# Kernel tuning notes

Measured on AMD Instinct MI355X. Metric: run time of the kernel, lower is better.

Reference implementation:

```python
import jax, jax.numpy as jnp
import numpy as np

N = 50000        # vertices
E = 1_600_000    # edges (avg degree 32)
CIN = 8          # in_channels (scalar input features)
COUT = 32        # out_channels (tangent vector channels, complex -> trailing dim 2)
R = 2            # n_corr_rings (radial profile rings)
EPS = 1e-6


def setup_inputs() -> dict:
    key = jax.random.key(0)
    ks = jax.random.split(key, 12)
    x = jax.random.normal(ks[0], (N, CIN), jnp.float32)
    edge_index = jax.random.randint(ks[1], (2, E), 0, N, dtype=jnp.int32)
    # precomputed per-edge transport * radial interpolation coefficients (re, im) per ring
    pcmp_gather = jax.random.normal(ks[2], (E, R, 2), jnp.float32)
    # TransField learned radial profile and phase offset (offset=True)
    W_rad = jax.random.normal(ks[3], (R, CIN, COUT), jnp.float32) / np.float32(np.sqrt(R * CIN))
    phase = jax.random.normal(ks[4], (COUT,), jnp.float32)
    # TangentNonLin bias after the field conv
    b_nl = jax.random.normal(ks[5], (COUT,), jnp.float32) * 0.1
    # three TangentPerceptrons: complex-linear (real weight shared over re/im) + TangentNonLin
    sc = np.float32(1.0 / np.sqrt(COUT))
    W1 = jax.random.normal(ks[6], (COUT, COUT), jnp.float32) * sc
    b1 = jax.random.normal(ks[7], (COUT,), jnp.float32) * 0.1
    W2 = jax.random.normal(ks[8], (COUT, COUT), jnp.float32) * sc
    b2 = jax.random.normal(ks[9], (COUT,), jnp.float32) * 0.1
    W3 = jax.random.normal(ks[10], (COUT, COUT), jnp.float32) * sc
    b3 = jax.random.normal(ks[11], (COUT,), jnp.float32) * 0.1
    return dict(x=x, edge_index=edge_index, pcmp_gather=pcmp_gather, W_rad=W_rad,
                phase=phase, b_nl=b_nl, W1=W1, b1=b1, W2=W2, b2=b2, W3=W3, b3=b3)


def tangent_nonlin(z, b):
    # ReLU on magnitude with learned per-channel bias, phase preserved
    mag = jnp.sqrt(jnp.sum(z * z, axis=-1) + EPS)           # [N, C]
    scale = jax.nn.relu(mag + b) / mag                      # [N, C]
    return z * scale[..., None]


def trans_field(x, src, dst, pcmp_gather, W_rad, phase, n_nodes):
    xs = x[src]                                             # gather: [E, CIN]
    t = jnp.einsum('ei,rio->ero', xs, W_rad)                # [E, R, COUT]
    # modulate by complex transport coeffs per ring, sum rings -> [E, COUT, 2]
    msg = jnp.sum(t[..., None] * pcmp_gather[:, :, None, :], axis=1)
    agg = jax.ops.segment_sum(msg, dst, num_segments=n_nodes)  # scatter: [N, COUT, 2]
    # learned phase offset: rotate each output channel by e^{i*phase}
    c, s = jnp.cos(phase), jnp.sin(phase)
    re = agg[..., 0] * c - agg[..., 1] * s
    im = agg[..., 0] * s + agg[..., 1] * c
    return jnp.stack([re, im], axis=-1)                     # [N, COUT, 2]


def reference(x, edge_index, pcmp_gather, W_rad, phase, b_nl, W1, b1, W2, b2, W3, b3):
    src, dst = edge_index[0], edge_index[1]
    y = trans_field(x, src, dst, pcmp_gather, W_rad, phase, x.shape[0])
    y = tangent_nonlin(y, b_nl)
    for W, b in ((W1, b1), (W2, b2), (W3, b3)):
        y = jnp.einsum('nik,io->nok', y, W)                 # complex-linear (shared real weight)
        y = tangent_nonlin(y, b)
    return y
```

## Files before the change

kernel.cpp:

```cpp
#include <hip/hip_runtime.h>

#define CIN 8
#define COUT 32
#define NR 2
#define EPSF 1e-6f

#define BSH 5
#define BNODES 32
#define NBMAX 2048
#define CHUNK 8192
#define IDBITS 21
#define IDMASK ((1u << IDBITS) - 1u)
#define SRCMASK 0x03FFFFFFu
#define PSTAGE 1792
#define AREG (PSTAGE / 256)

__global__ __launch_bounds__(256) void bucket_hist(
    const int* __restrict__ eidx, int* __restrict__ bucketCnt, int E, int nb)
{
    __shared__ int cnt[NBMAX];
    for (int i = threadIdx.x; i < nb; i += 256) cnt[i] = 0;
    __syncthreads();
    for (int e = blockIdx.x * 256 + threadIdx.x; e < E; e += gridDim.x * 256)
        atomicAdd(&cnt[eidx[E + e] >> BSH], 1);
    __syncthreads();
    for (int i = threadIdx.x; i < nb; i += 256)
        if (cnt[i]) atomicAdd(&bucketCnt[i], cnt[i]);
}

__global__ __launch_bounds__(1024) void scan_init(
    const int* __restrict__ bucketCnt, int* __restrict__ bucketBase,
    int* __restrict__ gCursor, int nb)
{
    __shared__ int sA[NBMAX], sB[NBMAX];
    for (int i = threadIdx.x; i < NBMAX; i += 1024)
        sA[i] = (i < nb) ? bucketCnt[i] : 0;
    __syncthreads();
    int* src = sA; int* dst = sB;
    for (int off = 1; off < NBMAX; off <<= 1) {
        for (int i = threadIdx.x; i < NBMAX; i += 1024)
            dst[i] = src[i] + (i >= off ? src[i - off] : 0);
        __syncthreads();
        int* tmp = src; src = dst; dst = tmp;
    }
    for (int i = threadIdx.x; i < nb; i += 1024) {
        int incl = src[i];
        int base = incl - bucketCnt[i];
        bucketBase[i] = base;
        gCursor[i] = base;
        if (i == nb - 1) bucketBase[nb] = incl;
    }
}

template<bool PACKED>
__global__ __launch_bounds__(256) void binify(
    const int* __restrict__ eidx, int* __restrict__ gCursor,
    unsigned* __restrict__ outMeta,
    float4*   __restrict__ pcmpS,
    const float* __restrict__ pcmp, int E, int nb)
{
    __shared__ int cnt[NBMAX];
    __shared__ int sA[NBMAX], sB[NBMAX];
    __shared__ int gbase[NBMAX];
    __shared__ unsigned sid[CHUNK];
    __shared__ unsigned short bucketOf[CHUNK];

    const int e0 = blockIdx.x * CHUNK;
    const int num = min(CHUNK, E - e0);

    for (int i = threadIdx.x; i < nb; i += 256) cnt[i] = 0;
    __syncthreads();
    for (int k = threadIdx.x; k < num; k += 256)
        atomicAdd(&cnt[eidx[E + e0 + k] >> BSH], 1);
    __syncthreads();

    for (int j = threadIdx.x; j < NBMAX; j += 256) sA[j] = (j < nb) ? cnt[j] : 0;
    __syncthreads();
    int* src = sA; int* dstp = sB;
    for (int off = 1; off < NBMAX; off <<= 1) {
        for (int j = threadIdx.x; j < NBMAX; j += 256)
            dstp[j] = src[j] + (j >= off ? src[j - off] : 0);
        __syncthreads();
        int* tmp = src; src = dstp; dstp = tmp;
    }

    for (int b = threadIdx.x; b < nb; b += 256)
        gbase[b] = atomicAdd(&gCursor[b], cnt[b]);
    __syncthreads();
    for (int i = threadIdx.x; i < nb; i += 256) cnt[i] = 0;
    __syncthreads();

    for (int k = threadIdx.x; k < num; k += 256) {
        int e = e0 + k;
        int d = eidx[E + e];
        int b = d >> BSH;
        int slot = (b ? src[b - 1] : 0) + atomicAdd(&cnt[b], 1);
        sid[slot] = ((unsigned)(d & (BNODES - 1)) << IDBITS) | (unsigned)e;
        bucketOf[slot] = (unsigned short)b;
    }
    __syncthreads();

    for (int s = threadIdx.x; s < num; s += 256) {
        int b = bucketOf[s];
        int intra = s - (b ? src[b - 1] : 0);
        unsigned v = sid[s];
        int pos = gbase[b] + intra;
        if (PACKED) {
            int id = v & IDMASK;
            unsigned dl = v >> IDBITS;
            unsigned sv = (unsigned)eidx[id];
            outMeta[pos] = (dl << 26) | sv;
            pcmpS[pos] = *reinterpret_cast<const float4*>(pcmp + (size_t)id * 4);
        } else {
            outMeta[pos] = v;
        }
    }
}

template<bool SRC16>
__global__ __launch_bounds__(256) void fused_team_kernel(
    const float* __restrict__ x,
    const float4* __restrict__ pcmpS,
    const unsigned* __restrict__ meta,
    const int* __restrict__ bucketBase,
    const float* __restrict__ W_rad, const float* __restrict__ phase,
    const float* __restrict__ b_nl,
    const float* __restrict__ W1, const float* __restrict__ b1,
    const float* __restrict__ W2, const float* __restrict__ b2,
    const float* __restrict__ W3, const float* __restrict__ b3,
    float* __restrict__ out, int N)
{
    __shared__ float sWrad[NR * CIN][COUT];
    __shared__ float sPh[COUT][2];
    __shared__ float sBias[4][COUT];
    __shared__ float4 pcL[PSTAGE];
    __shared__ unsigned short srcL16[SRC16 ? PSTAGE : 2];
    __shared__ unsigned srcL32[SRC16 ? 2 : PSTAGE];
    __shared__ float Qbuf[BNODES][33];
    __shared__ int cnt[BNODES], segS[BNODES], padL[BNODES], cur[BNODES];
    __shared__ int totPad;

    for (int i = threadIdx.x; i < NR * CIN * COUT; i += 256) ((float*)sWrad)[i] = W_rad[i];
    if (threadIdx.x < COUT) {
        float sn, cs; __sincosf(phase[threadIdx.x], &sn, &cs);
        sPh[threadIdx.x][0] = cs; sPh[threadIdx.x][1] = sn;
        sBias[0][threadIdx.x] = b_nl[threadIdx.x];
        sBias[1][threadIdx.x] = b1[threadIdx.x];
        sBias[2][threadIdx.x] = b2[threadIdx.x];
        sBias[3][threadIdx.x] = b3[threadIdx.x];
    }
    if (threadIdx.x < BNODES) cnt[threadIdx.x] = 0;

    const int start = bucketBase[blockIdx.x];
    const int total = bucketBase[blockIdx.x + 1] - start;
    const bool ovf0 = (total > PSTAGE);
    if (threadIdx.x == 0) totPad = ovf0 ? 0x7FFFFFFF : 0;
    __syncthreads();

    unsigned mreg[AREG];
    float4   preg[AREG];
    const int staged = ovf0 ? 0 : total;
#pragma unroll
    for (int kk = 0; kk < AREG; ++kk) {
        int k = threadIdx.x + (kk << 8);
        if (k < staged) {
            mreg[kk] = meta[start + k];
            preg[kk] = pcmpS[start + k];
            atomicAdd(&cnt[mreg[kk] >> 26], 1);
        }
    }
    __syncthreads();

    if (threadIdx.x < BNODES) {
        int v = cnt[threadIdx.x];
        int m = v;
        m = max(m, __shfl_xor(m, 1, 32));
        m = max(m, __shfl_xor(m, 2, 32));
        m = max(m, __shfl_xor(m, 4, 32));
        int pl = m;
        int incl = pl;
#pragma unroll
        for (int off = 1; off < BNODES; off <<= 1) {
            int u = __shfl_up(incl, off, 32);
            if ((int)threadIdx.x >= off) incl += u;
        }
        segS[threadIdx.x] = incl - pl;
        cur[threadIdx.x]  = incl - pl;
        padL[threadIdx.x] = pl;
        if (threadIdx.x == BNODES - 1 && !ovf0) totPad = incl;
    }
    __syncthreads();

    const bool fb = (totPad > PSTAGE);

    if (!fb) {
#pragma unroll
        for (int kk = 0; kk < AREG; ++kk) {
            int k = threadIdx.x + (kk << 8);
            if (k < staged) {
                unsigned m = mreg[kk];
                int pos = atomicAdd(&cur[m >> 26], 1);
                if (SRC16) srcL16[pos] = (unsigned short)(m & 0xFFFFu);
                else       srcL32[pos] = m & SRCMASK;
                pcL[pos] = preg[kk];
            }
        }
        if (threadIdx.x < BNODES) {
            int p0 = segS[threadIdx.x] + cnt[threadIdx.x];
            int p1 = segS[threadIdx.x] + padL[threadIdx.x];
            float4 z = {0.f, 0.f, 0.f, 0.f};
            for (int p = p0; p < p1; ++p) {
                if (SRC16) srcL16[p] = 0; else srcL32[p] = 0;
                pcL[p] = z;
            }
        }
    }
    __syncthreads();

    const int c    = threadIdx.x & 31;
    const int sub  = threadIdx.x >> 5;
    const int team = c >> 3;
    const int il   = c & 7;
    const int gl   = sub * 4 + team;
    const int node0 = blockIdx.x << BSH;

    float4 qa = {0.f, 0.f, 0.f, 0.f};
    if (!fb) {
        const int base = segS[gl];
        const int T = padL[gl];
#pragma unroll 4
        for (int t = 0; t < T; ++t) {
            int sv = SRC16 ? (int)srcL16[base + t] : (int)srcL32[base + t];
            float4 pc4 = pcL[base + t];
            float xf = x[(sv << 3) + il];
            qa.x += xf * pc4.x;
            qa.y += xf * pc4.y;
            qa.z += xf * pc4.z;
            qa.w += xf * pc4.w;
        }
    } else {
        const float4* pcG = pcmpS + start;
        for (int t = 0; t < total; ++t) {
            unsigned m = meta[start + t];
            if ((int)(m >> 26) == gl) {
                float4 pc4 = pcG[t];
                float xf = x[(size_t)(m & SRCMASK) * CIN + il];
                qa.x += xf * pc4.x;
                qa.y += xf * pc4.y;
                qa.z += xf * pc4.z;
                qa.w += xf * pc4.w;
            }
        }
    }

    Qbuf[gl][2 * il]      = qa.x;
    Qbuf[gl][2 * il + 1]  = qa.y;
    Qbuf[gl][16 + 2 * il] = qa.z;
    Qbuf[gl][17 + 2 * il] = qa.w;

    const float* __restrict__ Wt0 = W1;
    const float* __restrict__ Wt1 = W2;
    const float* __restrict__ Wt2 = W3;
#pragma unroll
    for (int r = 0; r < 4; ++r) {
        const int gln = sub * 4 + r;
        const int n   = node0 + gln;
        float a0 = 0.f, a1 = 0.f;
#pragma unroll
        for (int ri = 0; ri < NR * CIN; ++ri) {
            float w = sWrad[ri][c];
            a0 += w * Qbuf[gln][2 * ri];
            a1 += w * Qbuf[gln][2 * ri + 1];
        }
        float cs = sPh[c][0], sn = sPh[c][1];
        float re = a0 * cs - a1 * sn;
        float im = a0 * sn + a1 * cs;
        float mag = sqrtf(re * re + im * im + EPSF);
        float sc  = fmaxf(mag + sBias[0][c], 0.f) / mag;
        re *= sc; im *= sc;
#pragma unroll
        for (int L = 0; L < 3; ++L) {
            const float* __restrict__ Wl = (L == 0) ? Wt0 : (L == 1) ? Wt1 : Wt2;
            float bb0 = 0.f, bb1 = 0.f;
#pragma unroll
            for (int i = 0; i < COUT; ++i) {
                float w = Wl[i * COUT + c];
                bb0 += w * __shfl(re, i, 32);
                bb1 += w * __shfl(im, i, 32);
            }
            float m2 = sqrtf(bb0 * bb0 + bb1 * bb1 + EPSF);
            float s2 = fmaxf(m2 + sBias[L + 1][c], 0.f) / m2;
            re = bb0 * s2; im = bb1 * s2;
        }
        if (n < N) {
            float2 v; v.x = re; v.y = im;
            *reinterpret_cast<float2*>(out + ((n << 6) + (c << 1))) = v;
        }
    }
}

__global__ __launch_bounds__(256) void fused_bucket_fallback(
    const float* __restrict__ x, const int* __restrict__ eidx,
    const float* __restrict__ pcmp, const int* __restrict__ bucketBase,
    const unsigned* __restrict__ sorted,
    const float* __restrict__ W_rad, const float* __restrict__ phase,
    const float* __restrict__ b_nl,
    const float* __restrict__ W1, const float* __restrict__ b1,
    const float* __restrict__ W2, const float* __restrict__ b2,
    const float* __restrict__ W3, const float* __restrict__ b3,
    float* __restrict__ out, int N)
{
    __shared__ float Q[BNODES][COUT];
    __shared__ float sWrad[NR * CIN][COUT];
    __shared__ float sW[3][COUT][COUT];
    __shared__ float sPh[COUT][2];
    __shared__ float sBias[4][COUT];

    for (int i = threadIdx.x; i < BNODES * COUT; i += 256) ((float*)Q)[i] = 0.f;
    for (int i = threadIdx.x; i < NR * CIN * COUT; i += 256) ((float*)sWrad)[i] = W_rad[i];
    for (int i = threadIdx.x; i < COUT * COUT; i += 256) {
        ((float*)sW[0])[i] = W1[i];
        ((float*)sW[1])[i] = W2[i];
        ((float*)sW[2])[i] = W3[i];
    }
    if (threadIdx.x < COUT) {
        float sn, cs; __sincosf(phase[threadIdx.x], &sn, &cs);
        sPh[threadIdx.x][0] = cs; sPh[threadIdx.x][1] = sn;
        sBias[0][threadIdx.x] = b_nl[threadIdx.x];
        sBias[1][threadIdx.x] = b1[threadIdx.x];
        sBias[2][threadIdx.x] = b2[threadIdx.x];
        sBias[3][threadIdx.x] = b3[threadIdx.x];
    }
    __syncthreads();

    const int c   = threadIdx.x & 31;
    const int sub = threadIdx.x >> 5;
    const int i_idx  = (c >> 1) & 7;
    const int pc_off = ((c >> 4) << 1) | (c & 1);
    const int start = bucketBase[blockIdx.x];
    const int end   = bucketBase[blockIdx.x + 1];

    for (int p = start + sub; p < end; p += 8) {
        unsigned v0 = sorted[p];
        int id0 = v0 & IDMASK;
        int s0 = eidx[id0];
        atomicAdd(&Q[v0 >> IDBITS][c],
                  x[(size_t)s0 * CIN + i_idx] * pcmp[(size_t)id0 * 4 + pc_off]);
    }
    __syncthreads();

    const int node0 = blockIdx.x << BSH;
#pragma unroll
    for (int r = 0; r < 4; ++r) {
        const int gl = r * 8 + sub;
        const int n  = node0 + gl;
        float a0 = 0.f, a1 = 0.f;
#pragma unroll
        for (int ri = 0; ri < NR * CIN; ++ri) {
            float w = sWrad[ri][c];
            a0 += w * Q[gl][2 * ri];
            a1 += w * Q[gl][2 * ri + 1];
        }
        float cs = sPh[c][0], sn = sPh[c][1];
        float re = a0 * cs - a1 * sn;
        float im = a0 * sn + a1 * cs;
        float mag = sqrtf(re * re + im * im + EPSF);
        float sc  = fmaxf(mag + sBias[0][c], 0.f) / mag;
        re *= sc; im *= sc;
#pragma unroll
        for (int L = 0; L < 3; ++L) {
            float b0 = 0.f, b1v = 0.f;
#pragma unroll
            for (int i = 0; i < COUT; ++i) {
                float w = sW[L][i][c];
                b0  += w * __shfl(re, i, 32);
                b1v += w * __shfl(im, i, 32);
            }
            float m2 = sqrtf(b0 * b0 + b1v * b1v + EPSF);
            float s2 = fmaxf(m2 + sBias[L + 1][c], 0.f) / m2;
            re = b0 * s2; im = b1v * s2;
        }
        if (n < N) {
            float2 v; v.x = re; v.y = im;
            *reinterpret_cast<float2*>(out + ((size_t)n * COUT + c) * 2) = v;
        }
    }
}

extern "C" void kernel_launch(void* const* d_in, const int* in_sizes, int n_in,
                              void* d_out, int out_size, void* d_ws, size_t ws_size,
                              hipStream_t stream)
{
    const float* x     = (const float*)d_in[0];
    const int*   eidx  = (const int*)  d_in[1];
    const float* pcmp  = (const float*)d_in[2];
    const float* W_rad = (const float*)d_in[3];
    const float* phase = (const float*)d_in[4];
    const float* b_nl  = (const float*)d_in[5];
    const float* W1    = (const float*)d_in[6];
    const float* b1    = (const float*)d_in[7];
    const float* W2    = (const float*)d_in[8];
    const float* b2    = (const float*)d_in[9];
    const float* W3    = (const float*)d_in[10];
    const float* b3    = (const float*)d_in[11];
    float* out = (float*)d_out;

    const int N = in_sizes[0] / CIN;
    const int E = in_sizes[1] / 2;
    const int nb = (N + BNODES - 1) >> BSH;
    const int nchunk = (E + CHUNK - 1) / CHUNK;

    float4*   pcmpS      = (float4*)d_ws;
    unsigned* meta       = (unsigned*)(pcmpS + E);
    int*      bucketCnt  = (int*)(meta + E);
    int*      bucketBase = bucketCnt + NBMAX;
    int*      gCursor    = bucketBase + NBMAX + 1;
    size_t needed = (size_t)((char*)(gCursor + NBMAX) - (char*)d_ws);

    if (ws_size >= needed) {
        hipMemsetAsync(bucketCnt, 0, (size_t)nb * sizeof(int), stream);
        bucket_hist<<<256, 256, 0, stream>>>(eidx, bucketCnt, E, nb);
        scan_init<<<1, 1024, 0, stream>>>(bucketCnt, bucketBase, gCursor, nb);
        binify<true><<<nchunk, 256, 0, stream>>>(eidx, gCursor, meta, pcmpS, pcmp, E, nb);
        if (N <= 65536) {
            fused_team_kernel<true><<<nb, 256, 0, stream>>>(
                x, pcmpS, meta, bucketBase,
                W_rad, phase, b_nl, W1, b1, W2, b2, W3, b3, out, N);
        } else {
            fused_team_kernel<false><<<nb, 256, 0, stream>>>(
                x, pcmpS, meta, bucketBase,
                W_rad, phase, b_nl, W1, b1, W2, b2, W3, b3, out, N);
        }
    } else {
        int*      bc = (int*)d_ws;
        int*      bb = bc + NBMAX;
        int*      gc = bb + NBMAX + 1;
        unsigned* so = (unsigned*)(gc + NBMAX);
        hipMemsetAsync(bc, 0, (size_t)nb * sizeof(int), stream);
        bucket_hist<<<256, 256, 0, stream>>>(eidx, bc, E, nb);
        scan_init<<<1, 1024, 0, stream>>>(bc, bb, gc, nb);
        binify<false><<<nchunk, 256, 0, stream>>>(eidx, gc, so, nullptr, pcmp, E, nb);
        fused_bucket_fallback<<<nb, 256, 0, stream>>>(
            x, eidx, pcmp, bb, so,
            W_rad, phase, b_nl, W1, b1, W2, b2, W3, b3, out, N);
    }
}
```

Measured before the change: 182.9 us.

## Stage only packed indices in LDS and read pcmp from global to raise occupancy

The fused kernel no longer stages the float4 transport coefficients in shared memory or registers. It stores a packed (source, original-offset) word per sorted edge and reads pcmpS from global memory inside the aggregation loop, masking padded iterations instead of zero-filling padding. This cuts LDS use and register pressure so that launch_bounds(256,6) can keep more blocks resident, at the cost of scattered global float4 reads within a bucket. The binify kernel also moves to 512 threads with half-size chunks, which doubles the number of blocks.

After: 170.6 us. 6.7% less time.

```diff
diff --git a/kernel.cpp b/kernel.cpp
--- a/kernel.cpp
+++ b/kernel.cpp
@@ -8,7 +8,8 @@
 #define BSH 5
 #define BNODES 32
 #define NBMAX 2048
-#define CHUNK 8192
+#define CHUNK 4096
+#define BINT 512
 #define IDBITS 21
 #define IDMASK ((1u << IDBITS) - 1u)
 #define SRCMASK 0x03FFFFFFu
@@ -53,7 +54,7 @@
 }
 
 template<bool PACKED>
-__global__ __launch_bounds__(256) void binify(
+__global__ __launch_bounds__(BINT) void binify(
     const int* __restrict__ eidx, int* __restrict__ gCursor,
     unsigned* __restrict__ outMeta,
     float4*   __restrict__ pcmpS,
@@ -68,29 +69,29 @@
     const int e0 = blockIdx.x * CHUNK;
     const int num = min(CHUNK, E - e0);
 
-    for (int i = threadIdx.x; i < nb; i += 256) cnt[i] = 0;
-    __syncthreads();
-    for (int k = threadIdx.x; k < num; k += 256)
+    for (int i = threadIdx.x; i < nb; i += BINT) cnt[i] = 0;
+    __syncthreads();
+    for (int k = threadIdx.x; k < num; k += BINT)
         atomicAdd(&cnt[eidx[E + e0 + k] >> BSH], 1);
     __syncthreads();
 
-    for (int j = threadIdx.x; j < NBMAX; j += 256) sA[j] = (j < nb) ? cnt[j] : 0;
+    for (int j = threadIdx.x; j < NBMAX; j += BINT) sA[j] = (j < nb) ? cnt[j] : 0;
     __syncthreads();
     int* src = sA; int* dstp = sB;
     for (int off = 1; off < NBMAX; off <<= 1) {
-        for (int j = threadIdx.x; j < NBMAX; j += 256)
+        for (int j = threadIdx.x; j < NBMAX; j += BINT)
             dstp[j] = src[j] + (j >= off ? src[j - off] : 0);
         __syncthreads();
         int* tmp = src; src = dstp; dstp = tmp;
     }
 
-    for (int b = threadIdx.x; b < nb; b += 256)
+    for (int b = threadIdx.x; b < nb; b += BINT)
         gbase[b] = atomicAdd(&gCursor[b], cnt[b]);
     __syncthreads();
-    for (int i = threadIdx.x; i < nb; i += 256) cnt[i] = 0;
-    __syncthreads();
-
-    for (int k = threadIdx.x; k < num; k += 256) {
+    for (int i = threadIdx.x; i < nb; i += BINT) cnt[i] = 0;
+    __syncthreads();
+
+    for (int k = threadIdx.x; k < num; k += BINT) {
         int e = e0 + k;
         int d = eidx[E + e];
         int b = d >> BSH;
@@ -100,7 +101,7 @@
     }
     __syncthreads();
 
-    for (int s = threadIdx.x; s < num; s += 256) {
+    for (int s = threadIdx.x; s < num; s += BINT) {
         int b = bucketOf[s];
         int intra = s - (b ? src[b - 1] : 0);
         unsigned v = sid[s];
@@ -118,7 +119,7 @@
 }
 
 template<bool SRC16>
-__global__ __launch_bounds__(256) void fused_team_kernel(
+__global__ __launch_bounds__(256, 6) void fused_team_kernel(
     const float* __restrict__ x,
     const float4* __restrict__ pcmpS,
     const unsigned* __restrict__ meta,
@@ -133,12 +134,10 @@
     __shared__ float sWrad[NR * CIN][COUT];
     __shared__ float sPh[COUT][2];
     __shared__ float sBias[4][COUT];
-    __shared__ float4 pcL[PSTAGE];
-    __shared__ unsigned short srcL16[SRC16 ? PSTAGE : 2];
-    __shared__ unsigned srcL32[SRC16 ? 2 : PSTAGE];
+    __shared__ unsigned srtPk[PSTAGE];
+    __shared__ unsigned short srtK[SRC16 ? 2 : PSTAGE];
     __shared__ float Qbuf[BNODES][33];
     __shared__ int cnt[BNODES], segS[BNODES], padL[BNODES], cur[BNODES];
-    __shared__ int totPad;
 
     for (int i = threadIdx.x; i < NR * CIN * COUT; i += 256) ((float*)sWrad)[i] = W_rad[i];
     if (threadIdx.x < COUT) {
@@ -153,19 +152,16 @@
 
     const int start = bucketBase[blockIdx.x];
     const int total = bucketBase[blockIdx.x + 1] - start;
-    const bool ovf0 = (total > PSTAGE);
-    if (threadIdx.x == 0) totPad = ovf0 ? 0x7FFFFFFF : 0;
+    const bool fb = (total > PSTAGE);
     __syncthreads();
 
     unsigned mreg[AREG];
-    float4   preg[AREG];
-    const int staged = ovf0 ? 0 : total;
+    const int staged = fb ? 0 : total;
 #pragma unroll
     for (int kk = 0; kk < AREG; ++kk) {
         int k = threadIdx.x + (kk << 8);
         if (k < staged) {
             mreg[kk] = meta[start + k];
-            preg[kk] = pcmpS[start + k];
             atomicAdd(&cnt[mreg[kk] >> 26], 1);
         }
     }
@@ -177,21 +173,17 @@
         m = max(m, __shfl_xor(m, 1, 32));
         m = max(m, __shfl_xor(m, 2, 32));
         m = max(m, __shfl_xor(m, 4, 32));
-        int pl = m;
-        int incl = pl;
+        int incl = v;
 #pragma unroll
         for (int off = 1; off < BNODES; off <<= 1) {
             int u = __shfl_up(incl, off, 32);
             if ((int)threadIdx.x >= off) incl += u;
         }
-        segS[threadIdx.x] = incl - pl;
-        cur[threadIdx.x]  = incl - pl;
-        padL[threadIdx.x] = pl;
-        if (threadIdx.x == BNODES - 1 && !ovf0) totPad = incl;
-    }
-    __syncthreads();
-
-    const bool fb = (totPad > PSTAGE);
+        segS[threadIdx.x] = incl - v;
+        cur[threadIdx.x]  = incl - v;
+        padL[threadIdx.x] = m;
+    }
+    __syncthreads();
 
     if (!fb) {
 #pragma unroll
@@ -200,18 +192,12 @@
             if (k < staged) {
                 unsigned m = mreg[kk];
                 int pos = atomicAdd(&cur[m >> 26], 1);
-                if (SRC16) srcL16[pos] = (unsigned short)(m & 0xFFFFu);
-                else       srcL32[pos] = m & SRCMASK;
-                pcL[pos] = preg[kk];
-            }
-        }
-        if (threadIdx.x < BNODES) {
-            int p0 = segS[threadIdx.x] + cnt[threadIdx.x];
-            int p1 = segS[threadIdx.x] + padL[threadIdx.x];
-            float4 z = {0.f, 0.f, 0.f, 0.f};
-            for (int p = p0; p < p1; ++p) {
-                if (SRC16) srcL16[p] = 0; else srcL32[p] = 0;
-                pcL[p] = z;
+                if (SRC16) {
+                    srtPk[pos] = ((unsigned)k << 16) | (m & 0xFFFFu);
+                } else {
+                    srtPk[pos] = m & SRCMASK;
+                    srtK[pos] = (unsigned short)k;
+                }
             }
         }
     }
@@ -226,13 +212,23 @@
 
     float4 qa = {0.f, 0.f, 0.f, 0.f};
     if (!fb) {
-        const int base = segS[gl];
-        const int T = padL[gl];
+        const int base  = segS[gl];
+        const int myCnt = cnt[gl];
+        const int Tw    = padL[gl];
+        const int last  = total - 1;
 #pragma unroll 4
-        for (int t = 0; t < T; ++t) {
-            int sv = SRC16 ? (int)srcL16[base + t] : (int)srcL32[base + t];
-            float4 pc4 = pcL[base + t];
-            float xf = x[(sv << 3) + il];
+        for (int t = 0; t < Tw; ++t) {
+            bool act = (t < myCnt);
+            int slot = min(base + t, last);
+            int sv, kk2;
+            if (SRC16) {
+                unsigned p = srtPk[slot];
+                sv = (int)(p & 0xFFFFu); kk2 = (int)(p >> 16);
+            } else {
+                sv = (int)srtPk[slot]; kk2 = (int)srtK[slot];
+            }
+            float4 pc4 = pcmpS[start + kk2];
+            float xf = act ? x[(sv << 3) + il] : 0.f;
             qa.x += xf * pc4.x;
             qa.y += xf * pc4.y;
             qa.z += xf * pc4.z;
@@ -258,9 +254,6 @@
     Qbuf[gl][16 + 2 * il] = qa.z;
     Qbuf[gl][17 + 2 * il] = qa.w;
 
-    const float* __restrict__ Wt0 = W1;
-    const float* __restrict__ Wt1 = W2;
-    const float* __restrict__ Wt2 = W3;
 #pragma unroll
     for (int r = 0; r < 4; ++r) {
         const int gln = sub * 4 + r;
@@ -280,7 +273,7 @@
         re *= sc; im *= sc;
 #pragma unroll
         for (int L = 0; L < 3; ++L) {
-            const float* __restrict__ Wl = (L == 0) ? Wt0 : (L == 1) ? Wt1 : Wt2;
+            const float* __restrict__ Wl = (L == 0) ? W1 : (L == 1) ? W2 : W3;
             float bb0 = 0.f, bb1 = 0.f;
 #pragma unroll
             for (int i = 0; i < COUT; ++i) {
@@ -421,7 +414,7 @@
         hipMemsetAsync(bucketCnt, 0, (size_t)nb * sizeof(int), stream);
         bucket_hist<<<256, 256, 0, stream>>>(eidx, bucketCnt, E, nb);
         scan_init<<<1, 1024, 0, stream>>>(bucketCnt, bucketBase, gCursor, nb);
-        binify<true><<<nchunk, 256, 0, stream>>>(eidx, gCursor, meta, pcmpS, pcmp, E, nb);
+        binify<true><<<nchunk, BINT, 0, stream>>>(eidx, gCursor, meta, pcmpS, pcmp, E, nb);
         if (N <= 65536) {
             fused_team_kernel<true><<<nb, 256, 0, stream>>>(
                 x, pcmpS, meta, bucketBase,
@@ -439,7 +432,7 @@
         hipMemsetAsync(bc, 0, (size_t)nb * sizeof(int), stream);
         bucket_hist<<<256, 256, 0, stream>>>(eidx, bc, E, nb);
         scan_init<<<1, 1024, 0, stream>>>(bc, bb, gc, nb);
-        binify<false><<<nchunk, 256, 0, stream>>>(eidx, gc, so, nullptr, pcmp, E, nb);
+        binify<false><<<nchunk, BINT, 0, stream>>>(eidx, gc, so, nullptr, pcmp, E, nb);
         fused_bucket_fallback<<<nb, 256, 0, stream>>>(
             x, eidx, pcmp, bb, so,
             W_rad, phase, b_nl, W1, b1, W2, b2, W3, b3, out, N);
```
